# Kernel optimization log

Measured on AMD Instinct MI355X. Metric: run time of the kernel, lower is better.

## Reference

```python
import jax, jax.numpy as jnp
import numpy as np
import math

EMBED_DIM = 512
NUM_HEADS = 8
B, T = 1, 4096

def setup_inputs() -> dict:
    key = jax.random.key(0)
    ks = jax.random.split(key, 12)
    D = EMBED_DIM
    s = 1.0 / math.sqrt(D)
    inp = {
        "x": jax.random.normal(ks[0], (B, T, D), dtype=jnp.float32),
        "ln1_scale": jnp.ones((D,), jnp.float32),
        "ln1_bias": jnp.zeros((D,), jnp.float32),
        "Wq": jax.random.normal(ks[1], (D, D), jnp.float32) * s,
        "bq": jnp.zeros((D,), jnp.float32),
        "Wk": jax.random.normal(ks[2], (D, D), jnp.float32) * s,
        "bk": jnp.zeros((D,), jnp.float32),
        "Wv": jax.random.normal(ks[3], (D, D), jnp.float32) * s,
        "bv": jnp.zeros((D,), jnp.float32),
        "Wo": jax.random.normal(ks[4], (D, D), jnp.float32) * s,
        "bo": jnp.zeros((D,), jnp.float32),
        "ln2_scale": jnp.ones((D,), jnp.float32),
        "ln2_bias": jnp.zeros((D,), jnp.float32),
        "W1": jax.random.normal(ks[5], (D, 4 * D), jnp.float32) * s,
        "b1": jnp.zeros((4 * D,), jnp.float32),
        "W2": jax.random.normal(ks[6], (4 * D, D), jnp.float32) * (1.0 / math.sqrt(4 * D)),
        "b2": jnp.zeros((D,), jnp.float32),
    }
    return inp

def _layernorm(x, scale, bias, eps=1e-6):
    mu = jnp.mean(x, axis=-1, keepdims=True)
    var = jnp.mean(jnp.square(x - mu), axis=-1, keepdims=True)
    return (x - mu) * jax.lax.rsqrt(var + eps) * scale + bias

def reference(x, ln1_scale, ln1_bias, Wq, bq, Wk, bk, Wv, bv, Wo, bo,
              ln2_scale, ln2_bias, W1, b1, W2, b2):
    Bb, Tt, D = x.shape
    H = NUM_HEADS
    hd = D // H
    residual = x
    h = _layernorm(x, ln1_scale, ln1_bias)
    q = (h @ Wq + bq).reshape(Bb, Tt, H, hd).transpose(0, 2, 1, 3)
    k = (h @ Wk + bk).reshape(Bb, Tt, H, hd).transpose(0, 2, 1, 3)
    v = (h @ Wv + bv).reshape(Bb, Tt, H, hd).transpose(0, 2, 1, 3)
    # [B,H,T,T] scores (naive attention as in the original module)
    scores = jnp.einsum('bhqd,bhkd->bhqk', q, k) / math.sqrt(hd)
    probs = jax.nn.softmax(scores, axis=-1)
    out = jnp.einsum('bhqk,bhkd->bhqd', probs, v).transpose(0, 2, 1, 3).reshape(Bb, Tt, D)
    h = out @ Wo + bo  # dropout deterministic -> identity
    x = h + residual
    residual = x
    h = _layernorm(x, ln2_scale, ln2_bias)
    h = jax.nn.gelu(h @ W1 + b1, approximate=True)
    h = h @ W2 + b2
    return h + residual
```

## Files before the change

### kernel.cpp

```cpp
#include <hip/hip_runtime.h>
#include <hip/hip_bf16.h>
#include <stdint.h>

typedef __bf16 bf16;
typedef __bf16 bf16x4 __attribute__((ext_vector_type(4)));
typedef __bf16 bf16x8 __attribute__((ext_vector_type(8)));
typedef float  f32x4  __attribute__((ext_vector_type(4)));
typedef float  f32x16 __attribute__((ext_vector_type(16)));

#define MFMA32(A_, B_, C_) __builtin_amdgcn_mfma_f32_32x32x16_bf16((A_), (B_), (C_), 0, 0, 0)

#define QSCALE 0.1803368801111137f

__device__ __forceinline__ void gload_lds16(const void* g, void* l) {
  __builtin_amdgcn_global_load_lds(
      (const __attribute__((address_space(1))) unsigned int*)g,
      (__attribute__((address_space(3))) unsigned int*)l, 16, 0, 0);
}

__device__ __forceinline__ unsigned pk2(float lo, float hi_) {
  union { bf16 h[2]; unsigned u; } t;
  t.h[0] = (bf16)lo; t.h[1] = (bf16)hi_;
  return t.u;
}

__device__ __forceinline__ float fast_exp2(float x) {
#if __has_builtin(__builtin_amdgcn_exp2f)
  return __builtin_amdgcn_exp2f(x);
#else
  return exp2f(x);
#endif
}

__global__ __launch_bounds__(256) void prep_ln(const float* __restrict__ Wq,
                                               const float* __restrict__ Wk,
                                               const float* __restrict__ Wv,
                                               const float* __restrict__ Wo,
                                               const float* __restrict__ W1,
                                               const float* __restrict__ W2,
                                               const float* __restrict__ bq,
                                               const float* __restrict__ bk,
                                               const float* __restrict__ bv,
                                               bf16* __restrict__ wqkvT, bf16* __restrict__ woT,
                                               bf16* __restrict__ w1T, bf16* __restrict__ w2T,
                                               float* __restrict__ bqkv,
                                               const float* __restrict__ x,
                                               const float* __restrict__ ln1s,
                                               const float* __restrict__ ln1b,
                                               bf16* __restrict__ h) {
  const int b = blockIdx.x;
  if (b >= 774) {
    const int w = threadIdx.x >> 6, l = threadIdx.x & 63;
    const int row = (b - 774) * 4 + w;
    const float4* xp = (const float4*)(x + (size_t)row * 512 + l * 8);
    float4 v0 = xp[0], v1 = xp[1];
    float xv[8] = {v0.x, v0.y, v0.z, v0.w, v1.x, v1.y, v1.z, v1.w};
    float s = 0.f, q = 0.f;
#pragma unroll
    for (int j = 0; j < 8; ++j) { s += xv[j]; q += xv[j] * xv[j]; }
#pragma unroll
    for (int m = 1; m < 64; m <<= 1) { s += __shfl_xor(s, m); q += __shfl_xor(q, m); }
    const float mean = s * (1.f / 512.f);
    const float var = q * (1.f / 512.f) - mean * mean;
    const float rstd = rsqrtf(var + 1e-6f);
    const float4* scp = (const float4*)(ln1s + l * 8);
    const float4* bip = (const float4*)(ln1b + l * 8);
    float4 s0 = scp[0], s1 = scp[1], b0 = bip[0], b1 = bip[1];
    float sv[8] = {s0.x, s0.y, s0.z, s0.w, s1.x, s1.y, s1.z, s1.w};
    float bvv[8] = {b0.x, b0.y, b0.z, b0.w, b1.x, b1.y, b1.z, b1.w};
    bf16x8 ov;
#pragma unroll
    for (int j = 0; j < 8; ++j) ov[j] = (bf16)((xv[j] - mean) * rstd * sv[j] + bvv[j]);
    *(bf16x8*)(h + (size_t)row * 512 + l * 8) = ov;
    return;
  }
  if (b >= 768) {
    int i = (b - 768) * 256 + threadIdx.x;
    if (i < 1536)
      bqkv[i] = (i < 512) ? bq[i] * QSCALE : (i < 1024 ? bk[i - 512] : bv[i - 1024]);
    return;
  }
  const float* in; bf16* outp; int K, N, t; float sc = 1.f;
  if (b < 64)       { in = Wq; outp = wqkvT;              K = 512;  N = 512;  t = b;       sc = QSCALE; }
  else if (b < 128) { in = Wk; outp = wqkvT + 512 * 512;  K = 512;  N = 512;  t = b - 64;  }
  else if (b < 192) { in = Wv; outp = wqkvT + 1024 * 512; K = 512;  N = 512;  t = b - 128; }
  else if (b < 256) { in = Wo; outp = woT;                K = 512;  N = 512;  t = b - 192; }
  else if (b < 512) { in = W1; outp = w1T;                K = 512;  N = 2048; t = b - 256; }
  else              { in = W2; outp = w2T;                K = 2048; N = 512;  t = b - 512; }
  const int tx = K >> 6;
  const int k0 = (t % tx) * 64, n0 = (t / tx) * 64;
  __shared__ bf16 tile[64][72];
  const int tid = threadIdx.x;
#pragma unroll
  for (int s = 0; s < 16; ++s) {
    int j = tid + s * 256;
    int r = j >> 6, c = j & 63;
    tile[r][c] = (bf16)(in[(size_t)(k0 + r) * N + n0 + c] * sc);
  }
  __syncthreads();
#pragma unroll
  for (int s = 0; s < 16; ++s) {
    int j = tid + s * 256;
    int n = j >> 6, k = j & 63;
    outp[(size_t)(n0 + n) * K + k0 + k] = tile[k][n];
  }
}

__global__ __launch_bounds__(256) void ln2_comb(const bf16* __restrict__ p0,
                                                const bf16* __restrict__ p1,
                                                const float* __restrict__ x,
                                                const float* __restrict__ bo,
                                                const float* __restrict__ sc,
                                                const float* __restrict__ bi,
                                                float* __restrict__ x2,
                                                bf16* __restrict__ h2) {
  const int w = threadIdx.x >> 6, l = threadIdx.x & 63;
  const int row = blockIdx.x * 4 + w;
  const size_t base = (size_t)row * 512 + l * 8;
  bf16x8 a = *(const bf16x8*)(p0 + base);
  bf16x8 b = *(const bf16x8*)(p1 + base);
  float xv[8];
#pragma unroll
  for (int j = 0; j < 2; ++j) {
    float4 c = *(const float4*)(x + base + j * 4);
    float4 d = *(const float4*)(bo + l * 8 + j * 4);
    xv[j * 4 + 0] = (float)a[j * 4 + 0] + (float)b[j * 4 + 0] + c.x + d.x;
    xv[j * 4 + 1] = (float)a[j * 4 + 1] + (float)b[j * 4 + 1] + c.y + d.y;
    xv[j * 4 + 2] = (float)a[j * 4 + 2] + (float)b[j * 4 + 2] + c.z + d.z;
    xv[j * 4 + 3] = (float)a[j * 4 + 3] + (float)b[j * 4 + 3] + c.w + d.w;
  }
  *(float4*)(x2 + base) = make_float4(xv[0], xv[1], xv[2], xv[3]);
  *(float4*)(x2 + base + 4) = make_float4(xv[4], xv[5], xv[6], xv[7]);
  float s = 0.f, q = 0.f;
#pragma unroll
  for (int j = 0; j < 8; ++j) { s += xv[j]; q += xv[j] * xv[j]; }
#pragma unroll
  for (int m = 1; m < 64; m <<= 1) { s += __shfl_xor(s, m); q += __shfl_xor(q, m); }
  const float mean = s * (1.f / 512.f);
  const float var = q * (1.f / 512.f) - mean * mean;
  const float rstd = rsqrtf(var + 1e-6f);
  const float4* scp = (const float4*)(sc + l * 8);
  const float4* bip = (const float4*)(bi + l * 8);
  float4 s0 = scp[0], s1 = scp[1], b0 = bip[0], b1 = bip[1];
  float sv[8] = {s0.x, s0.y, s0.z, s0.w, s1.x, s1.y, s1.z, s1.w};
  float bvv[8] = {b0.x, b0.y, b0.z, b0.w, b1.x, b1.y, b1.z, b1.w};
  bf16x8 ov;
#pragma unroll
  for (int j = 0; j < 8; ++j) ov[j] = (bf16)((xv[j] - mean) * rstd * sv[j] + bvv[j]);
  *(bf16x8*)(h2 + base) = ov;
}

__global__ __launch_bounds__(256) void final_comb(const bf16* __restrict__ parts, int nsplit,
                                                  const float* __restrict__ b2,
                                                  const float* __restrict__ x2,
                                                  float* __restrict__ outp) {
  const int i8 = blockIdx.x * 256 + threadIdx.x;
  const size_t off = (size_t)i8 * 8;
  float acc[8];
  float4 xa = *(const float4*)(x2 + off);
  float4 xb = *(const float4*)(x2 + off + 4);
  float4 ba = *(const float4*)(b2 + (off & 511));
  float4 bb = *(const float4*)(b2 + ((off & 511) + 4));
  acc[0] = xa.x + ba.x; acc[1] = xa.y + ba.y; acc[2] = xa.z + ba.z; acc[3] = xa.w + ba.w;
  acc[4] = xb.x + bb.x; acc[5] = xb.y + bb.y; acc[6] = xb.z + bb.z; acc[7] = xb.w + bb.w;
  for (int z = 0; z < nsplit; ++z) {
    bf16x8 p = *(const bf16x8*)(parts + (size_t)z * 2097152 + off);
#pragma unroll
    for (int j = 0; j < 8; ++j) acc[j] += (float)p[j];
  }
  *(float4*)(outp + off) = make_float4(acc[0], acc[1], acc[2], acc[3]);
  *(float4*)(outp + off + 4) = make_float4(acc[4], acc[5], acc[6], acc[7]);
}

template <int EPI>
__global__ __launch_bounds__(256, 4) void gemm32(const bf16* __restrict__ A,
                                                 const bf16* __restrict__ Bt,
                                                 const float* __restrict__ bias,
                                                 const float* __restrict__ res,
                                                 void* __restrict__ outp,
                                                 bf16* __restrict__ k2,
                                                 bf16* __restrict__ vd,
                                                 int M, int N, int K) {
  __shared__ bf16 a_lds[2][64 * 64];
  __shared__ bf16 b_lds[2][64 * 64];
  const int m0 = blockIdx.x * 64, n0 = blockIdx.y * 64;
  const int tid = threadIdx.x, l = tid & 63, w = tid >> 6;
  const int wm = w >> 1, wn = w & 1;
  const int hi = l >> 5, l5 = l & 31;
  const int lr = l >> 3;
  const int cs = (l & 7) ^ (lr & 7);
  const int swl = l5 & 7;

  const bf16* ag = A + (size_t)(m0 + w * 16 + lr) * K + cs * 8;
  const bf16* bg = Bt + (size_t)(n0 + w * 16 + lr) * K + cs * 8;
  const size_t r8 = (size_t)8 * K;

#define GS32(B_)                                                   \
  do {                                                             \
    gload_lds16(ag,      (char*)a_lds[B_] + (w * 16) * 128);       \
    gload_lds16(ag + r8, (char*)a_lds[B_] + (w * 16 + 8) * 128);   \
    gload_lds16(bg,      (char*)b_lds[B_] + (w * 16) * 128);       \
    gload_lds16(bg + r8, (char*)b_lds[B_] + (w * 16 + 8) * 128);   \
    ag += 64; bg += 64;                                            \
  } while (0)

  f32x16 acc = {};
  const int kiters = K >> 6;
  GS32(0);
  __syncthreads();
  for (int kt = 0; kt < kiters; ++kt) {
    const int cur = kt & 1;
    if (kt + 1 < kiters) GS32(cur ^ 1);
    const bf16* ab = a_lds[cur] + (wm * 32 + l5) * 64;
    const bf16* bb = b_lds[cur] + (wn * 32 + l5) * 64;
#pragma unroll
    for (int kk = 0; kk < 4; ++kk) {
      bf16x8 af = *(const bf16x8*)(ab + ((kk * 2 + hi) ^ swl) * 8);
      bf16x8 bf_ = *(const bf16x8*)(bb + ((kk * 2 + hi) ^ swl) * 8);
      acc = MFMA32(bf_, af, acc);
    }
    __syncthreads();
  }
#undef GS32

  const int row = m0 + wm * 32 + l5;
#pragma unroll
  for (int rg = 0; rg < 4; ++rg) {
    const int cb = n0 + wn * 32 + rg * 8 + hi * 4;
    float4 bb4 = *(const float4*)(bias + cb);
    float v[4];
    v[0] = acc[rg * 4 + 0] + bb4.x;
    v[1] = acc[rg * 4 + 1] + bb4.y;
    v[2] = acc[rg * 4 + 2] + bb4.z;
    v[3] = acc[rg * 4 + 3] + bb4.w;
    if constexpr (EPI == 1) {
      float4 rr = *(const float4*)(res + (size_t)row * N + cb);
      *(float4*)((float*)outp + (size_t)row * N + cb) =
          make_float4(v[0] + rr.x, v[1] + rr.y, v[2] + rr.z, v[3] + rr.w);
    } else if constexpr (EPI == 2) {
      bf16x4 o;
#pragma unroll
      for (int e = 0; e < 4; ++e) {
        float t = -2.3022077697f * (v[e] + 0.044715f * v[e] * v[e] * v[e]);
        o[e] = (bf16)(v[e] / (1.f + fast_exp2(t)));
      }
      *(bf16x4*)((bf16*)outp + (size_t)row * N + cb) = o;
    } else {
      bf16x4 o;
#pragma unroll
      for (int e = 0; e < 4; ++e) o[e] = (bf16)v[e];
      if (n0 < 512) {
        *(bf16x4*)((bf16*)outp + (size_t)row * 512 + cb) = o;
      } else if (n0 < 1024) {
        const int hd = (n0 - 512) >> 6, d = cb & 63;
        *(bf16x4*)(k2 + (size_t)hd * 262144 + (size_t)row * 64 + d) = o;
      } else {
        const int hd = (n0 - 1024) >> 6, d = cb & 63;
        *(bf16x4*)(vd + (size_t)hd * 262144 + (size_t)row * 64 + d) = o;
      }
    }
  }
}

__global__ __launch_bounds__(256, 4) void gemm32_skp(const bf16* __restrict__ A,
                                                     const bf16* __restrict__ Bt,
                                                     bf16* __restrict__ parts,
                                                     int M, int N, int Kstride, int Kc) {
  __shared__ bf16 a_lds[2][64 * 64];
  __shared__ bf16 b_lds[2][64 * 64];
  const int m0 = blockIdx.x * 64, n0 = blockIdx.y * 64, kz = blockIdx.z;
  A += (size_t)kz * Kc;
  Bt += (size_t)kz * Kc;
  bf16* outp = parts + (size_t)kz * M * N;
  const int tid = threadIdx.x, l = tid & 63, w = tid >> 6;
  const int wm = w >> 1, wn = w & 1;
  const int hi = l >> 5, l5 = l & 31;
  const int lr = l >> 3;
  const int cs = (l & 7) ^ (lr & 7);
  const int swl = l5 & 7;

  const bf16* ag = A + (size_t)(m0 + w * 16 + lr) * Kstride + cs * 8;
  const bf16* bg = Bt + (size_t)(n0 + w * 16 + lr) * Kstride + cs * 8;
  const size_t r8 = (size_t)8 * Kstride;

#define GS32(B_)                                                   \
  do {                                                             \
    gload_lds16(ag,      (char*)a_lds[B_] + (w * 16) * 128);       \
    gload_lds16(ag + r8, (char*)a_lds[B_] + (w * 16 + 8) * 128);   \
    gload_lds16(bg,      (char*)b_lds[B_] + (w * 16) * 128);       \
    gload_lds16(bg + r8, (char*)b_lds[B_] + (w * 16 + 8) * 128);   \
    ag += 64; bg += 64;                                            \
  } while (0)

  f32x16 acc = {};
  const int kiters = Kc >> 6;
  GS32(0);
  __syncthreads();
  for (int kt = 0; kt < kiters; ++kt) {
    const int cur = kt & 1;
    if (kt + 1 < kiters) GS32(cur ^ 1);
    const bf16* ab = a_lds[cur] + (wm * 32 + l5) * 64;
    const bf16* bb = b_lds[cur] + (wn * 32 + l5) * 64;
#pragma unroll
    for (int kk = 0; kk < 4; ++kk) {
      bf16x8 af = *(const bf16x8*)(ab + ((kk * 2 + hi) ^ swl) * 8);
      bf16x8 bf_ = *(const bf16x8*)(bb + ((kk * 2 + hi) ^ swl) * 8);
      acc = MFMA32(bf_, af, acc);
    }
    __syncthreads();
  }
#undef GS32

  const int row = m0 + wm * 32 + l5;
#pragma unroll
  for (int rg = 0; rg < 4; ++rg) {
    const int cb = n0 + wn * 32 + rg * 8 + hi * 4;
    bf16x4 o;
#pragma unroll
    for (int e = 0; e < 4; ++e) o[e] = (bf16)acc[rg * 4 + e];
    *(bf16x4*)(outp + (size_t)row * N + cb) = o;
  }
}

__global__ __launch_bounds__(256) void vtrans(const bf16* __restrict__ vd,
                                              bf16* __restrict__ v2) {
  __shared__ bf16 tile[64][72];
  const int t0 = blockIdx.x * 64;
  const int head = blockIdx.y;
  const int tid = threadIdx.x;
#pragma unroll
  for (int s = 0; s < 16; ++s) {
    int j = tid + s * 256;
    int t = j >> 6, d = j & 63;
    tile[t][d] = vd[(size_t)head * 262144 + (size_t)(t0 + t) * 64 + d];
  }
  __syncthreads();
#pragma unroll
  for (int s = 0; s < 16; ++s) {
    int j = tid + s * 256;
    int d = j >> 6, t = j & 63;
    v2[(size_t)head * 262144 + (size_t)((t0 >> 5) + (t >> 5)) * 2048 + d * 32 + (t & 31)] =
        tile[t][d];
  }
}

__global__ __launch_bounds__(256, 4) void attn_k(const bf16* __restrict__ q2,
                                                 const bf16* __restrict__ k2,
                                                 const bf16* __restrict__ v2,
                                                 bf16* __restrict__ opart,
                                                 float* __restrict__ lpart) {
  const int bid = blockIdx.x;
  const int head = bid & 7;
  const int qt = (bid >> 3) & 63;
  const int ks = bid >> 9;
  const int w = threadIdx.x >> 6, l = threadIdx.x & 63;
  const int hi = l >> 5, l5 = l & 31;
  const int pair = w >> 1, wq = w & 1;

  __shared__ __align__(16) char smem[32768];
  char* kt_l = smem + pair * 16384;
  char* vt_l = kt_l + 8192;

  const int qrow0 = qt * 64 + wq * 32;
  const bf16* qb = q2 + (size_t)(qrow0 + l5) * 512 + head * 64;
  bf16x8 qf[4];
#pragma unroll
  for (int cc = 0; cc < 4; ++cc) qf[cc] = *(const bf16x8*)(qb + cc * 16 + hi * 8);

  const int kstart = ks * 2048 + pair * 1024;

  const int lr = l >> 3;
  const int lc3 = (l & 7) ^ lr;
  const char* kg = (const char*)k2 + (size_t)head * 524288 + (size_t)kstart * 128 +
                   (wq * 16 + lr) * 128 + lc3 * 16;
  const char* vg = (const char*)v2 + (size_t)head * 524288 + (size_t)(kstart >> 5) * 4096 +
                   (lc3 >> 2) * 2048 + (wq * 16 + lr) * 64 + (lc3 & 3) * 16;
  const int kdst = wq * 2048;

#define STAGE(B_)                                                            \
  do {                                                                       \
    gload_lds16(kg,        kt_l + (B_) * 4096 + kdst);                       \
    gload_lds16(kg + 1024, kt_l + (B_) * 4096 + kdst + 1024);                \
    gload_lds16(vg,        vt_l + (B_) * 4096 + kdst);                       \
    gload_lds16(vg + 512,  vt_l + (B_) * 4096 + kdst + 1024);                \
    kg += 4096; vg += 4096;                                                  \
  } while (0)

  STAGE(0);
  __syncthreads();

  f32x16 o0 = {}, o1 = {};
  float psum = 0.f;
  const int swl = l5 & 7;
  const char* kbase = kt_l + l5 * 128;
  const char* vbase = vt_l + l5 * 128;

  for (int t = 0; t < 32; ++t) {
    const int cur = t & 1;
    if (t < 31) STAGE(cur ^ 1);

    __builtin_amdgcn_s_setprio(1);
    f32x16 s = {};
#pragma unroll
    for (int cc = 0; cc < 4; ++cc) {
      bf16x8 kf = *(const bf16x8*)(kbase + cur * 4096 + ((cc * 2 + hi) ^ swl) * 16);
      s = MFMA32(kf, qf[cc], s);
    }
    __builtin_amdgcn_s_setprio(0);

#pragma unroll
    for (int c = 0; c < 2; ++c) {
      float p[8];
#pragma unroll
      for (int j = 0; j < 8; ++j) p[j] = fast_exp2(s[c * 8 + j]);
      psum += ((p[0] + p[1]) + (p[2] + p[3])) + ((p[4] + p[5]) + (p[6] + p[7]));
      unsigned X = pk2(p[0], p[1]), X2 = pk2(p[2], p[3]);
      unsigned Y = pk2(p[4], p[5]), Y2 = pk2(p[6], p[7]);
      asm volatile("v_permlane32_swap_b32 %0, %1" : "+v"(X), "+v"(Y));
      asm volatile("v_permlane32_swap_b32 %0, %1" : "+v"(X2), "+v"(Y2));
      union { unsigned wd[4]; bf16x8 v; } pa;
      pa.wd[0] = X; pa.wd[1] = X2; pa.wd[2] = Y; pa.wd[3] = Y2;
      bf16x8 vf0 = *(const bf16x8*)(vbase + cur * 4096 + ((c * 2 + hi) ^ swl) * 16);
      bf16x8 vf1 = *(const bf16x8*)(vbase + cur * 4096 + ((4 + c * 2 + hi) ^ swl) * 16);
      __builtin_amdgcn_s_setprio(1);
      o0 = MFMA32(vf0, pa.v, o0);
      o1 = MFMA32(vf1, pa.v, o1);
      __builtin_amdgcn_s_setprio(0);
    }
    __syncthreads();
  }
#undef STAGE

  float* comb = (float*)smem;
  if (w >= 2) {
    float* cb = comb + ((w - 2) * 64 + l) * 33;
#pragma unroll
    for (int r = 0; r < 16; ++r) { cb[r] = o0[r]; cb[16 + r] = o1[r]; }
    cb[32] = psum;
  }
  __syncthreads();
  if (w < 2) {
    const float* cb = comb + (w * 64 + l) * 33;
#pragma unroll
    for (int r = 0; r < 16; ++r) { o0[r] += cb[r]; o1[r] += cb[16 + r]; }
    psum += cb[32];
    const float lsum = psum + __shfl_xor(psum, 32);
    bf16* ob = opart + (size_t)ks * 4096 * 512 + (size_t)(qrow0 + l5) * 512 + head * 64;
#pragma unroll
    for (int dt = 0; dt < 2; ++dt)
#pragma unroll
      for (int rg = 0; rg < 4; ++rg) {
        bf16x4 vv;
#pragma unroll
        for (int e = 0; e < 4; ++e) {
          const float ov = (dt == 0) ? o0[rg * 4 + e] : o1[rg * 4 + e];
          vv[e] = (bf16)ov;
        }
        *(bf16x4*)(ob + dt * 32 + rg * 8 + hi * 4) = vv;
      }
    if (hi == 0) lpart[(ks * 8 + head) * 4096 + qrow0 + l5] = lsum;
  }
}

__global__ __launch_bounds__(256) void attn_comb(const bf16* __restrict__ op,
                                                 const float* __restrict__ lp,
                                                 bf16* __restrict__ ob) {
  const int idx = blockIdx.x * 256 + threadIdx.x;
  const int t = idx >> 6, c8 = idx & 63;
  const int head = c8 >> 3;
  const size_t o = (size_t)t * 512 + c8 * 8;
  bf16x8 a = *(const bf16x8*)(op + o);
  bf16x8 b = *(const bf16x8*)(op + 2097152 + o);
  const float inv = 1.f / (lp[head * 4096 + t] + lp[32768 + head * 4096 + t]);
  bf16x8 r;
#pragma unroll
  for (int j = 0; j < 8; ++j) r[j] = (bf16)(((float)a[j] + (float)b[j]) * inv);
  *(bf16x8*)(ob + o) = r;
}

extern "C" void kernel_launch(void* const* d_in, const int* in_sizes, int n_in,
                              void* d_out, int out_size, void* d_ws, size_t ws_size,
                              hipStream_t stream) {
  const float* x    = (const float*)d_in[0];
  const float* ln1s = (const float*)d_in[1];
  const float* ln1b = (const float*)d_in[2];
  const float* Wq   = (const float*)d_in[3];
  const float* bq   = (const float*)d_in[4];
  const float* Wk   = (const float*)d_in[5];
  const float* bk   = (const float*)d_in[6];
  const float* Wv   = (const float*)d_in[7];
  const float* bv   = (const float*)d_in[8];
  const float* Wo   = (const float*)d_in[9];
  const float* bo   = (const float*)d_in[10];
  const float* ln2s = (const float*)d_in[11];
  const float* ln2b = (const float*)d_in[12];
  const float* W1   = (const float*)d_in[13];
  const float* b1   = (const float*)d_in[14];
  const float* W2   = (const float*)d_in[15];
  const float* b2   = (const float*)d_in[16];
  float* out = (float*)d_out;

  char* ws = (char*)d_ws;
  bf16*  wqkvT = (bf16*)(ws + 0);
  bf16*  woT   = (bf16*)(ws + 1572864);
  bf16*  w1T   = (bf16*)(ws + 2097152);
  bf16*  w2T   = (bf16*)(ws + 4194304);
  float* bqkv  = (float*)(ws + 6291456);
  float* lpart = (float*)(ws + 6299648);
  bf16*  opart = (bf16*)(ws + 6561792);
  float* x2    = (float*)(ws + 6561792);
  bf16*  h     = (bf16*)(ws + 14950400);
  bf16*  q2    = (bf16*)(ws + 19144704);
  bf16*  k2    = (bf16*)(ws + 23339008);
  bf16*  v2    = (bf16*)(ws + 27533312);
  bf16*  vd    = (bf16*)(ws + 31727616);
  bf16*  attnb = h;
  bf16*  h2    = h;
  bf16*  wop   = (bf16*)(ws + 19144704);
  bf16*  gbuf  = (bf16*)(ws + 19144704);
  bf16*  f2p   = (bf16*)(ws + 35921920);
  const size_t need4 = 35921920 + 4ull * 4194304;
  const size_t need2 = 35921920 + 2ull * 4194304;

  prep_ln<<<1798, 256, 0, stream>>>(Wq, Wk, Wv, Wo, W1, W2, bq, bk, bv,
                                    wqkvT, woT, w1T, w2T, bqkv, x, ln1s, ln1b, h);
  gemm32<3><<<dim3(64, 24), 256, 0, stream>>>(h, wqkvT, bqkv, nullptr, q2, k2, vd,
                                              4096, 1536, 512);
  vtrans<<<dim3(64, 8), 256, 0, stream>>>(vd, v2);
  attn_k<<<1024, 256, 0, stream>>>(q2, k2, v2, opart, lpart);
  attn_comb<<<1024, 256, 0, stream>>>(opart, lpart, attnb);
  gemm32_skp<<<dim3(64, 8, 2), 256, 0, stream>>>(attnb, woT, wop, 4096, 512, 512, 256);
  ln2_comb<<<1024, 256, 0, stream>>>(wop, wop + 2097152, x, bo, ln2s, ln2b, x2, h2);
  gemm32<2><<<dim3(64, 32), 256, 0, stream>>>(h2, w1T, b1, nullptr, gbuf, nullptr, nullptr,
                                              4096, 2048, 512);
  if (ws_size >= need4) {
    gemm32_skp<<<dim3(64, 8, 4), 256, 0, stream>>>(gbuf, w2T, f2p, 4096, 512, 2048, 512);
    final_comb<<<1024, 256, 0, stream>>>(f2p, 4, b2, x2, out);
  } else if (ws_size >= need2) {
    gemm32_skp<<<dim3(64, 8, 2), 256, 0, stream>>>(gbuf, w2T, f2p, 4096, 512, 2048, 1024);
    final_comb<<<1024, 256, 0, stream>>>(f2p, 2, b2, x2, out);
  } else {
    gemm32<1><<<dim3(64, 8), 256, 0, stream>>>(gbuf, w2T, b2, x2, out, nullptr, nullptr,
                                               4096, 512, 2048);
  }
}
```

Measured before the change: 150.8 us.

## Triple-buffer GEMM loads, fuse V transpose into QKV epilogue, merge attention split-K

```diff
diff --git a/kernel.cpp b/kernel.cpp
--- a/kernel.cpp
+++ b/kernel.cpp
@@ -173,16 +173,16 @@
 }
 
 template <int EPI>
-__global__ __launch_bounds__(256, 4) void gemm32(const bf16* __restrict__ A,
+__global__ __launch_bounds__(256, 3) void gemm32(const bf16* __restrict__ A,
                                                  const bf16* __restrict__ Bt,
                                                  const float* __restrict__ bias,
                                                  const float* __restrict__ res,
                                                  void* __restrict__ outp,
                                                  bf16* __restrict__ k2,
-                                                 bf16* __restrict__ vd,
+                                                 bf16* __restrict__ v2,
                                                  int M, int N, int K) {
-  __shared__ bf16 a_lds[2][64 * 64];
-  __shared__ bf16 b_lds[2][64 * 64];
+  __shared__ bf16 a_lds[3][64 * 64];
+  __shared__ bf16 b_lds[3][64 * 64];
   const int m0 = blockIdx.x * 64, n0 = blockIdx.y * 64;
   const int tid = threadIdx.x, l = tid & 63, w = tid >> 6;
   const int wm = w >> 1, wn = w & 1;
@@ -197,77 +197,114 @@
 
 #define GS32(B_)                                                   \
   do {                                                             \
-    gload_lds16(ag,      (char*)a_lds[B_] + (w * 16) * 128);       \
-    gload_lds16(ag + r8, (char*)a_lds[B_] + (w * 16 + 8) * 128);   \
-    gload_lds16(bg,      (char*)b_lds[B_] + (w * 16) * 128);       \
-    gload_lds16(bg + r8, (char*)b_lds[B_] + (w * 16 + 8) * 128);   \
+    gload_lds16(ag,      (char*)a_lds[(B_)] + (w * 16) * 128);     \
+    gload_lds16(ag + r8, (char*)a_lds[(B_)] + (w * 16 + 8) * 128); \
+    gload_lds16(bg,      (char*)b_lds[(B_)] + (w * 16) * 128);     \
+    gload_lds16(bg + r8, (char*)b_lds[(B_)] + (w * 16 + 8) * 128); \
     ag += 64; bg += 64;                                            \
   } while (0)
 
   f32x16 acc = {};
   const int kiters = K >> 6;
   GS32(0);
-  __syncthreads();
+  GS32(1);
+  asm volatile("s_waitcnt vmcnt(4)" ::: "memory");
+  __builtin_amdgcn_s_barrier();
   for (int kt = 0; kt < kiters; ++kt) {
-    const int cur = kt & 1;
-    if (kt + 1 < kiters) GS32(cur ^ 1);
-    const bf16* ab = a_lds[cur] + (wm * 32 + l5) * 64;
-    const bf16* bb = b_lds[cur] + (wn * 32 + l5) * 64;
+    if (kt + 2 < kiters) GS32((kt + 2) % 3);
+    const bf16* ab = a_lds[kt % 3] + (wm * 32 + l5) * 64;
+    const bf16* bb = b_lds[kt % 3] + (wn * 32 + l5) * 64;
 #pragma unroll
     for (int kk = 0; kk < 4; ++kk) {
       bf16x8 af = *(const bf16x8*)(ab + ((kk * 2 + hi) ^ swl) * 8);
       bf16x8 bf_ = *(const bf16x8*)(bb + ((kk * 2 + hi) ^ swl) * 8);
       acc = MFMA32(bf_, af, acc);
     }
+    if (kt + 1 < kiters) {
+      if (kt + 2 < kiters) asm volatile("s_waitcnt vmcnt(4)" ::: "memory");
+      else                 asm volatile("s_waitcnt vmcnt(0)" ::: "memory");
+      __builtin_amdgcn_s_barrier();
+    }
+  }
+#undef GS32
+
+  const int row = m0 + wm * 32 + l5;
+  if constexpr (EPI == 1 || EPI == 2) {
+#pragma unroll
+    for (int rg = 0; rg < 4; ++rg) {
+      const int cb = n0 + wn * 32 + rg * 8 + hi * 4;
+      float4 bb4 = *(const float4*)(bias + cb);
+      float v[4];
+      v[0] = acc[rg * 4 + 0] + bb4.x;
+      v[1] = acc[rg * 4 + 1] + bb4.y;
+      v[2] = acc[rg * 4 + 2] + bb4.z;
+      v[3] = acc[rg * 4 + 3] + bb4.w;
+      if constexpr (EPI == 1) {
+        float4 rr = *(const float4*)(res + (size_t)row * N + cb);
+        *(float4*)((float*)outp + (size_t)row * N + cb) =
+            make_float4(v[0] + rr.x, v[1] + rr.y, v[2] + rr.z, v[3] + rr.w);
+      } else {
+        bf16x4 o;
+#pragma unroll
+        for (int e = 0; e < 4; ++e) {
+          float t = -2.3022077697f * (v[e] + 0.044715f * v[e] * v[e] * v[e]);
+          o[e] = (bf16)(v[e] / (1.f + fast_exp2(t)));
+        }
+        *(bf16x4*)((bf16*)outp + (size_t)row * N + cb) = o;
+      }
+    }
+  } else {
     __syncthreads();
-  }
-#undef GS32
-
-  const int row = m0 + wm * 32 + l5;
-#pragma unroll
-  for (int rg = 0; rg < 4; ++rg) {
-    const int cb = n0 + wn * 32 + rg * 8 + hi * 4;
-    float4 bb4 = *(const float4*)(bias + cb);
-    float v[4];
-    v[0] = acc[rg * 4 + 0] + bb4.x;
-    v[1] = acc[rg * 4 + 1] + bb4.y;
-    v[2] = acc[rg * 4 + 2] + bb4.z;
-    v[3] = acc[rg * 4 + 3] + bb4.w;
-    if constexpr (EPI == 1) {
-      float4 rr = *(const float4*)(res + (size_t)row * N + cb);
-      *(float4*)((float*)outp + (size_t)row * N + cb) =
-          make_float4(v[0] + rr.x, v[1] + rr.y, v[2] + rr.z, v[3] + rr.w);
-    } else if constexpr (EPI == 2) {
+    bf16(*ct)[72] = (bf16(*)[72])a_lds;
+    const int rl = wm * 32 + l5;
+#pragma unroll
+    for (int rg = 0; rg < 4; ++rg) {
+      const int cl = wn * 32 + rg * 8 + hi * 4;
+      float4 bb4 = *(const float4*)(bias + n0 + cl);
       bf16x4 o;
-#pragma unroll
-      for (int e = 0; e < 4; ++e) {
-        float t = -2.3022077697f * (v[e] + 0.044715f * v[e] * v[e] * v[e]);
-        o[e] = (bf16)(v[e] / (1.f + fast_exp2(t)));
+      o[0] = (bf16)(acc[rg * 4 + 0] + bb4.x);
+      o[1] = (bf16)(acc[rg * 4 + 1] + bb4.y);
+      o[2] = (bf16)(acc[rg * 4 + 2] + bb4.z);
+      o[3] = (bf16)(acc[rg * 4 + 3] + bb4.w);
+      *(bf16x4*)(&ct[rl][cl]) = o;
+    }
+    __syncthreads();
+    if (n0 < 512) {
+#pragma unroll
+      for (int p = 0; p < 2; ++p) {
+        int idx = p * 256 + tid;
+        int r = idx >> 3, c = (idx & 7) * 8;
+        *(bf16x8*)((bf16*)outp + (size_t)(m0 + r) * 512 + n0 + c) =
+            *(const bf16x8*)(&ct[r][c]);
       }
-      *(bf16x4*)((bf16*)outp + (size_t)row * N + cb) = o;
+    } else if (n0 < 1024) {
+      bf16* kb = k2 + (size_t)((n0 - 512) >> 6) * 262144 + (size_t)m0 * 64;
+#pragma unroll
+      for (int p = 0; p < 2; ++p) {
+        int idx = p * 256 + tid;
+        int r = idx >> 3, c = (idx & 7) * 8;
+        *(bf16x8*)(kb + r * 64 + c) = *(const bf16x8*)(&ct[r][c]);
+      }
     } else {
-      bf16x4 o;
-#pragma unroll
-      for (int e = 0; e < 4; ++e) o[e] = (bf16)v[e];
-      if (n0 < 512) {
-        *(bf16x4*)((bf16*)outp + (size_t)row * 512 + cb) = o;
-      } else if (n0 < 1024) {
-        const int hd = (n0 - 512) >> 6, d = cb & 63;
-        *(bf16x4*)(k2 + (size_t)hd * 262144 + (size_t)row * 64 + d) = o;
-      } else {
-        const int hd = (n0 - 1024) >> 6, d = cb & 63;
-        *(bf16x4*)(vd + (size_t)hd * 262144 + (size_t)row * 64 + d) = o;
+      bf16* vb = v2 + (size_t)((n0 - 1024) >> 6) * 262144 + (size_t)(m0 >> 5) * 2048;
+      const int d = tid >> 2, t8 = (tid & 3) * 8;
+#pragma unroll
+      for (int p = 0; p < 2; ++p) {
+        bf16x8 vv;
+#pragma unroll
+        for (int e = 0; e < 8; ++e) vv[e] = ct[p * 32 + t8 + e][d];
+        *(bf16x8*)(vb + p * 2048 + d * 32 + t8) = vv;
       }
     }
   }
 }
 
-__global__ __launch_bounds__(256, 4) void gemm32_skp(const bf16* __restrict__ A,
+__global__ __launch_bounds__(256, 3) void gemm32_skp(const bf16* __restrict__ A,
                                                      const bf16* __restrict__ Bt,
                                                      bf16* __restrict__ parts,
                                                      int M, int N, int Kstride, int Kc) {
-  __shared__ bf16 a_lds[2][64 * 64];
-  __shared__ bf16 b_lds[2][64 * 64];
+  __shared__ bf16 a_lds[3][64 * 64];
+  __shared__ bf16 b_lds[3][64 * 64];
   const int m0 = blockIdx.x * 64, n0 = blockIdx.y * 64, kz = blockIdx.z;
   A += (size_t)kz * Kc;
   Bt += (size_t)kz * Kc;
@@ -285,29 +322,34 @@
 
 #define GS32(B_)                                                   \
   do {                                                             \
-    gload_lds16(ag,      (char*)a_lds[B_] + (w * 16) * 128);       \
-    gload_lds16(ag + r8, (char*)a_lds[B_] + (w * 16 + 8) * 128);   \
-    gload_lds16(bg,      (char*)b_lds[B_] + (w * 16) * 128);       \
-    gload_lds16(bg + r8, (char*)b_lds[B_] + (w * 16 + 8) * 128);   \
+    gload_lds16(ag,      (char*)a_lds[(B_)] + (w * 16) * 128);     \
+    gload_lds16(ag + r8, (char*)a_lds[(B_)] + (w * 16 + 8) * 128); \
+    gload_lds16(bg,      (char*)b_lds[(B_)] + (w * 16) * 128);     \
+    gload_lds16(bg + r8, (char*)b_lds[(B_)] + (w * 16 + 8) * 128); \
     ag += 64; bg += 64;                                            \
   } while (0)
 
   f32x16 acc = {};
   const int kiters = Kc >> 6;
   GS32(0);
-  __syncthreads();
+  GS32(1);
+  asm volatile("s_waitcnt vmcnt(4)" ::: "memory");
+  __builtin_amdgcn_s_barrier();
   for (int kt = 0; kt < kiters; ++kt) {
-    const int cur = kt & 1;
-    if (kt + 1 < kiters) GS32(cur ^ 1);
-    const bf16* ab = a_lds[cur] + (wm * 32 + l5) * 64;
-    const bf16* bb = b_lds[cur] + (wn * 32 + l5) * 64;
+    if (kt + 2 < kiters) GS32((kt + 2) % 3);
+    const bf16* ab = a_lds[kt % 3] + (wm * 32 + l5) * 64;
+    const bf16* bb = b_lds[kt % 3] + (wn * 32 + l5) * 64;
 #pragma unroll
     for (int kk = 0; kk < 4; ++kk) {
       bf16x8 af = *(const bf16x8*)(ab + ((kk * 2 + hi) ^ swl) * 8);
       bf16x8 bf_ = *(const bf16x8*)(bb + ((kk * 2 + hi) ^ swl) * 8);
       acc = MFMA32(bf_, af, acc);
     }
-    __syncthreads();
+    if (kt + 1 < kiters) {
+      if (kt + 2 < kiters) asm volatile("s_waitcnt vmcnt(4)" ::: "memory");
+      else                 asm volatile("s_waitcnt vmcnt(0)" ::: "memory");
+      __builtin_amdgcn_s_barrier();
+    }
   }
 #undef GS32
 
@@ -322,42 +364,18 @@
   }
 }
 
-__global__ __launch_bounds__(256) void vtrans(const bf16* __restrict__ vd,
-                                              bf16* __restrict__ v2) {
-  __shared__ bf16 tile[64][72];
-  const int t0 = blockIdx.x * 64;
-  const int head = blockIdx.y;
-  const int tid = threadIdx.x;
-#pragma unroll
-  for (int s = 0; s < 16; ++s) {
-    int j = tid + s * 256;
-    int t = j >> 6, d = j & 63;
-    tile[t][d] = vd[(size_t)head * 262144 + (size_t)(t0 + t) * 64 + d];
-  }
-  __syncthreads();
-#pragma unroll
-  for (int s = 0; s < 16; ++s) {
-    int j = tid + s * 256;
-    int d = j >> 6, t = j & 63;
-    v2[(size_t)head * 262144 + (size_t)((t0 >> 5) + (t >> 5)) * 2048 + d * 32 + (t & 31)] =
-        tile[t][d];
-  }
-}
-
-__global__ __launch_bounds__(256, 4) void attn_k(const bf16* __restrict__ q2,
+__global__ __launch_bounds__(512, 4) void attn_k(const bf16* __restrict__ q2,
                                                  const bf16* __restrict__ k2,
                                                  const bf16* __restrict__ v2,
-                                                 bf16* __restrict__ opart,
-                                                 float* __restrict__ lpart) {
+                                                 bf16* __restrict__ attnb) {
   const int bid = blockIdx.x;
   const int head = bid & 7;
-  const int qt = (bid >> 3) & 63;
-  const int ks = bid >> 9;
+  const int qt = bid >> 3;
   const int w = threadIdx.x >> 6, l = threadIdx.x & 63;
   const int hi = l >> 5, l5 = l & 31;
   const int pair = w >> 1, wq = w & 1;
 
-  __shared__ __align__(16) char smem[32768];
+  __shared__ __align__(16) char smem[65536];
   char* kt_l = smem + pair * 16384;
   char* vt_l = kt_l + 8192;
 
@@ -367,7 +385,7 @@
 #pragma unroll
   for (int cc = 0; cc < 4; ++cc) qf[cc] = *(const bf16x8*)(qb + cc * 16 + hi * 8);
 
-  const int kstart = ks * 2048 + pair * 1024;
+  const int kstart = pair * 1024;
 
   const int lr = l >> 3;
   const int lc3 = (l & 7) ^ lr;
@@ -432,20 +450,24 @@
 #undef STAGE
 
   float* comb = (float*)smem;
-  if (w >= 2) {
-    float* cb = comb + ((w - 2) * 64 + l) * 33;
+  if (pair > 0) {
+    float* cb = comb + (((pair - 1) * 2 + wq) * 64 + l) * 33;
 #pragma unroll
     for (int r = 0; r < 16; ++r) { cb[r] = o0[r]; cb[16 + r] = o1[r]; }
     cb[32] = psum;
   }
   __syncthreads();
-  if (w < 2) {
-    const float* cb = comb + (w * 64 + l) * 33;
-#pragma unroll
-    for (int r = 0; r < 16; ++r) { o0[r] += cb[r]; o1[r] += cb[16 + r]; }
-    psum += cb[32];
+  if (pair == 0) {
+#pragma unroll
+    for (int p = 0; p < 3; ++p) {
+      const float* cb = comb + ((p * 2 + wq) * 64 + l) * 33;
+#pragma unroll
+      for (int r = 0; r < 16; ++r) { o0[r] += cb[r]; o1[r] += cb[16 + r]; }
+      psum += cb[32];
+    }
     const float lsum = psum + __shfl_xor(psum, 32);
-    bf16* ob = opart + (size_t)ks * 4096 * 512 + (size_t)(qrow0 + l5) * 512 + head * 64;
+    const float inv = 1.f / lsum;
+    bf16* ob = attnb + (size_t)(qrow0 + l5) * 512 + head * 64;
 #pragma unroll
     for (int dt = 0; dt < 2; ++dt)
 #pragma unroll
@@ -454,28 +476,11 @@
 #pragma unroll
         for (int e = 0; e < 4; ++e) {
           const float ov = (dt == 0) ? o0[rg * 4 + e] : o1[rg * 4 + e];
-          vv[e] = (bf16)ov;
+          vv[e] = (bf16)(ov * inv);
         }
         *(bf16x4*)(ob + dt * 32 + rg * 8 + hi * 4) = vv;
       }
-    if (hi == 0) lpart[(ks * 8 + head) * 4096 + qrow0 + l5] = lsum;
-  }
-}
-
-__global__ __launch_bounds__(256) void attn_comb(const bf16* __restrict__ op,
-                                                 const float* __restrict__ lp,
-                                                 bf16* __restrict__ ob) {
-  const int idx = blockIdx.x * 256 + threadIdx.x;
-  const int t = idx >> 6, c8 = idx & 63;
-  const int head = c8 >> 3;
-  const size_t o = (size_t)t * 512 + c8 * 8;
-  bf16x8 a = *(const bf16x8*)(op + o);
-  bf16x8 b = *(const bf16x8*)(op + 2097152 + o);
-  const float inv = 1.f / (lp[head * 4096 + t] + lp[32768 + head * 4096 + t]);
-  bf16x8 r;
-#pragma unroll
-  for (int j = 0; j < 8; ++j) r[j] = (bf16)(((float)a[j] + (float)b[j]) * inv);
-  *(bf16x8*)(ob + o) = r;
+  }
 }
 
 extern "C" void kernel_launch(void* const* d_in, const int* in_sizes, int n_in,
@@ -506,29 +511,24 @@
   bf16*  w1T   = (bf16*)(ws + 2097152);
   bf16*  w2T   = (bf16*)(ws + 4194304);
   float* bqkv  = (float*)(ws + 6291456);
-  float* lpart = (float*)(ws + 6299648);
-  bf16*  opart = (bf16*)(ws + 6561792);
-  float* x2    = (float*)(ws + 6561792);
-  bf16*  h     = (bf16*)(ws + 14950400);
-  bf16*  q2    = (bf16*)(ws + 19144704);
-  bf16*  k2    = (bf16*)(ws + 23339008);
-  bf16*  v2    = (bf16*)(ws + 27533312);
-  bf16*  vd    = (bf16*)(ws + 31727616);
+  float* x2    = (float*)(ws + 6297600);
+  bf16*  h     = (bf16*)(ws + 14686208);
+  bf16*  q2    = (bf16*)(ws + 18880512);
+  bf16*  k2    = (bf16*)(ws + 23074816);
+  bf16*  v2    = (bf16*)(ws + 27269120);
   bf16*  attnb = h;
   bf16*  h2    = h;
-  bf16*  wop   = (bf16*)(ws + 19144704);
-  bf16*  gbuf  = (bf16*)(ws + 19144704);
-  bf16*  f2p   = (bf16*)(ws + 35921920);
-  const size_t need4 = 35921920 + 4ull * 4194304;
-  const size_t need2 = 35921920 + 2ull * 4194304;
+  bf16*  wop   = (bf16*)(ws + 18880512);
+  bf16*  gbuf  = (bf16*)(ws + 18880512);
+  bf16*  f2p   = (bf16*)(ws + 35657728);
+  const size_t need4 = 35657728 + 4ull * 4194304;
+  const size_t need2 = 35657728 + 2ull * 4194304;
 
   prep_ln<<<1798, 256, 0, stream>>>(Wq, Wk, Wv, Wo, W1, W2, bq, bk, bv,
                                     wqkvT, woT, w1T, w2T, bqkv, x, ln1s, ln1b, h);
-  gemm32<3><<<dim3(64, 24), 256, 0, stream>>>(h, wqkvT, bqkv, nullptr, q2, k2, vd,
+  gemm32<3><<<dim3(64, 24), 256, 0, stream>>>(h, wqkvT, bqkv, nullptr, q2, k2, v2,
                                               4096, 1536, 512);
-  vtrans<<<dim3(64, 8), 256, 0, stream>>>(vd, v2);
-  attn_k<<<1024, 256, 0, stream>>>(q2, k2, v2, opart, lpart);
-  attn_comb<<<1024, 256, 0, stream>>>(opart, lpart, attnb);
+  attn_k<<<512, 512, 0, stream>>>(q2, k2, v2, attnb);
   gemm32_skp<<<dim3(64, 8, 2), 256, 0, stream>>>(attnb, woT, wop, 4096, 512, 512, 256);
   ln2_comb<<<1024, 256, 0, stream>>>(wop, wop + 2097152, x, bo, ln2s, ln2b, x2, h2);
   gemm32<2><<<dim3(64, 32), 256, 0, stream>>>(h2, w1T, b1, nullptr, gbuf, nullptr, nullptr,
```

After: 146.8 us. 1.03x faster.
